# Optimization experiments

Measured on AMD Instinct MI355X. Metric: run time of the kernel, lower is better.

Reference implementation:

```python
import jax, jax.numpy as jnp
import numpy as np

N_NODES = 100000


def _segment_mean(h, src, dst, n_nodes):
    # copy_u: gather source features along edges, then mean-reduce per dst node
    msg = h[src]                                             # [E, D]
    s = jax.ops.segment_sum(msg, dst, num_segments=n_nodes)  # [N, D]
    cnt = jax.ops.segment_sum(jnp.ones((src.shape[0],), h.dtype), dst,
                              num_segments=n_nodes)          # [N]
    return s / jnp.maximum(cnt, 1.0)[:, None]


def setup_inputs() -> dict:
    key = jax.random.key(0)
    k1, k2, k3, k4, k5 = jax.random.split(key, 5)
    in_feats, n_hidden, n_classes = 128, 128, 64
    n_edges = 1600000
    features = jax.random.normal(k1, (N_NODES, in_feats), dtype=jnp.float32)
    W1 = jax.random.normal(k2, (in_feats, n_hidden), dtype=jnp.float32) * (1.0 / np.sqrt(in_feats))
    b1 = jnp.zeros((n_hidden,), jnp.float32)
    W2 = jax.random.normal(k3, (n_hidden, n_classes), dtype=jnp.float32) * (1.0 / np.sqrt(n_hidden))
    b2 = jnp.zeros((n_classes,), jnp.float32)
    src = jax.random.randint(k4, (n_edges,), 0, N_NODES, dtype=jnp.int64)
    dst = jax.random.randint(k5, (n_edges,), 0, N_NODES, dtype=jnp.int64)
    return {"features": features, "W1": W1, "b1": b1, "W2": W2, "b2": b2,
            "src": src, "dst": dst}


def reference(features, W1, b1, W2, b2, src, dst):
    # Layer 0: mean aggregation -> Linear -> relu  (dropout p=0.0 is identity)
    h = _segment_mean(features, src, dst, N_NODES)
    h = jax.nn.relu(h @ W1 + b1)
    # Layer 1: mean aggregation -> Linear (no activation on output layer)
    h = _segment_mean(h, src, dst, N_NODES)
    h = h @ W2 + b2
    return h
```

## Files before the change

kernel.cpp:

```cpp
#include <hip/hip_runtime.h>

#define N_NODES 100000
#define D 128
#define NE 1600000
#define C_OUT 64
#define NB 391
#define SENT 100000
#define P2B 256
#define P2E 6250
#define SEGSTRIDE 6400

typedef _Float16 half8 __attribute__((ext_vector_type(8)));
typedef float floatx4 __attribute__((ext_vector_type(4)));


__device__ inline half8 shfl_xor_h8(half8 v, int mask) {
    union { half8 h; int i[4]; } u;
    u.h = v;
    u.i[0] = __shfl_xor(u.i[0], mask);
    u.i[1] = __shfl_xor(u.i[1], mask);
    u.i[2] = __shfl_xor(u.i[2], mask);
    u.i[3] = __shfl_xor(u.i[3], mask);
    return u.h;
}

__device__ inline void pack_one(const float* W, _Float16* Wp, int tid, int N) {
    int l = tid & 63, p = tid >> 6;
    int nt = p >> 2, kc = p & 3;
    int quad = l >> 4, c = l & 15;
    int n = nt * 16 + c;
    half8 h;
    #pragma unroll
    for (int j = 0; j < 8; ++j) {
        int k = kc * 32 + quad * 8 + j;
        h[j] = (_Float16)W[k * N + n];
    }
    *(half8*)(Wp + (size_t)p * 512 + l * 8) = h;
}

__global__ __launch_bounds__(1024) void k1_p2_setup(const int* __restrict__ src,
                                                    const int* __restrict__ dst,
                                                    unsigned* __restrict__ gwords,
                                                    int* __restrict__ ofsg,
                                                    const float* __restrict__ W1,
                                                    const float* __restrict__ W2,
                                                    _Float16* __restrict__ wp1,
                                                    _Float16* __restrict__ wp2,
                                                    int* __restrict__ t1s,
                                                    int* __restrict__ t2s) {
    if (blockIdx.x >= P2B) {
        const int blk = blockIdx.x - P2B;
        const int t = threadIdx.x;
        if (t < 256) {
            if (blk < 8) {
                pack_one(W1, wp1, blk * 256 + t, 128);
            } else if (blk < 12) {
                pack_one(W2, wp2, (blk - 8) * 256 + t, 64);
            } else {
                if (t < 64) t1s[t] = 0;
                else if (t < 96) t2s[t - 64] = 0;
            }
        }
        return;
    }

    __shared__ unsigned ebuf[P2E];
    __shared__ int hist[NB];
    __shared__ int ofs[NB + 1];
    __shared__ int cur[NB];
    __shared__ int wsum[8];
    const int t = threadIdx.x;
    const int base = blockIdx.x * P2E;

    for (int i = t; i < NB; i += 1024) hist[i] = 0;
    __syncthreads();

    unsigned w[7];
    int bk[7];
    #pragma unroll
    for (int r = 0; r < 7; ++r) {
        const int j = r * 1024 + t;
        if (j < P2E) {
            const int e = base + j;
            const int d = dst[e];
            w[r] = ((unsigned)(d & 255) << 20) | (unsigned)src[e];
            bk[r] = d >> 8;
            atomicAdd(&hist[bk[r]], 1);
        } else {
            bk[r] = -1;
        }
    }
    __syncthreads();

    int v = 0, incl = 0;
    if (t < 512) { v = (t < NB) ? hist[t] : 0; incl = v; }
    #pragma unroll
    for (int d = 1; d < 64; d <<= 1) {
        int y = __shfl_up(incl, d);
        if ((t & 63) >= d) incl += y;
    }
    if (t < 512 && (t & 63) == 63) wsum[t >> 6] = incl;
    __syncthreads();
    if (t < NB) {
        int ex = incl - v;
        const int wv = t >> 6;
        for (int j = 0; j < wv; ++j) ex += wsum[j];
        ofs[t] = ex;
        cur[t] = ex;
    }
    if (t == 0) ofs[NB] = P2E;
    __syncthreads();

    #pragma unroll
    for (int r = 0; r < 7; ++r) {
        if (bk[r] >= 0) {
            const int slot = atomicAdd(&cur[bk[r]], 1);
            ebuf[slot] = w[r];
        }
    }
    __syncthreads();

    unsigned* gout = gwords + (size_t)blockIdx.x * SEGSTRIDE;
    for (int i = t; i < P2E; i += 1024) gout[i] = ebuf[i];
    int* oout = ofsg + blockIdx.x * (NB + 1);
    for (int i = t; i < NB + 1; i += 1024) oout[i] = ofs[i];
}

__global__ __launch_bounds__(256) void k2_p3_gemm1(const unsigned* __restrict__ gwords,
                                                   const int* __restrict__ ofsg,
                                                   int* __restrict__ ptrp,
                                                   int* __restrict__ pcnt,
                                                   float* __restrict__ inv,
                                                   int* __restrict__ csr,
                                                   const float* __restrict__ A,
                                                   const _Float16* __restrict__ Wp,
                                                   _Float16* __restrict__ outh) {
    __shared__ __align__(16) char smem[40960];
    const int t = threadIdx.x;

    if (blockIdx.x < NB) {
        unsigned* wbuf = (unsigned*)smem;
        int* sa   = (int*)(smem + 32768);
        int* sl   = (int*)(smem + 33792);
        int* so   = (int*)(smem + 34816);
        int* lcnt = (int*)(smem + 35840);
        int* lofs = (int*)(smem + 36864);
        int* ws4  = (int*)(smem + 37888);
        const int b = blockIdx.x;
        const int lane = t & 63, wave = t >> 6;

        const int* row = ofsg + t * (NB + 1);
        const int a0 = row[b];
        const int len = row[b + 1] - a0;
        sa[t] = a0;
        sl[t] = len;

        int sv = a0;
        #pragma unroll
        for (int m2 = 1; m2 < 64; m2 <<= 1) sv += __shfl_xor(sv, m2);
        if (lane == 0) ws4[wave] = sv;
        __syncthreads();
        const int pad_base = (ws4[0] + ws4[1] + ws4[2] + ws4[3]) + 1792 * b;
        __syncthreads();

        int incl = len;
        #pragma unroll
        for (int d = 1; d < 64; d <<= 1) {
            int y = __shfl_up(incl, d);
            if (lane >= d) incl += y;
        }
        if (lane == 63) ws4[wave] = incl;
        lcnt[t] = 0;
        __syncthreads();
        int off = incl - len;
        for (int j = 0; j < wave; ++j) off += ws4[j];
        so[t] = off;
        const int tot = min(ws4[0] + ws4[1] + ws4[2] + ws4[3], 8192);
        __syncthreads();

        const int grp = t >> 4, gl = t & 15;
        for (int seg = grp; seg < P2B; seg += 16) {
            const int sega = sa[seg];
            const int segl = sl[seg];
            const int sego = so[seg];
            if (sego + segl > 8192) continue;
            const unsigned* sp = gwords + (size_t)seg * SEGSTRIDE + sega;
            for (int j = gl; j < segl; j += 16) {
                const unsigned w = sp[j];
                wbuf[sego + j] = w;
                atomicAdd(&lcnt[(w >> 20) & 255], 1);
            }
        }
        __syncthreads();

        const int v = lcnt[t];
        const int pc = (v + 7) & ~7;
        int incl2 = pc;
        #pragma unroll
        for (int d = 1; d < 64; d <<= 1) {
            int y = __shfl_up(incl2, d);
            if (lane >= d) incl2 += y;
        }
        __syncthreads();
        if (lane == 63) ws4[wave] = incl2;
        __syncthreads();
        int ex = incl2 - pc;
        for (int j = 0; j < wave; ++j) ex += ws4[j];

        const int node = b * 256 + t;
        if (node < N_NODES) {
            ptrp[node] = pad_base + ex;
            pcnt[node] = pc;
            inv[node] = 1.0f / fmaxf((float)v, 1.0f);
        }
        for (int j = v; j < pc; ++j) csr[pad_base + ex + j] = SENT;

        __syncthreads();
        lofs[t] = ex;
        __syncthreads();
        for (int i = t; i < tot; i += 256) {
            const unsigned w = wbuf[i];
            const int pos = atomicAdd(&lofs[(w >> 20) & 255], 1);
            csr[pad_base + pos] = (int)(w & 0xFFFFF);
        }
        return;
    }

    _Float16* Wl = (_Float16*)smem;
    _Float16* Al = (_Float16*)(smem + 32768);
    {
        const floatx4* s4 = (const floatx4*)Wp;
        floatx4* d4 = (floatx4*)Wl;
        #pragma unroll
        for (int i = 0; i < 8; ++i) d4[t + 256 * i] = s4[t + 256 * i];
    }
    const int lane = t & 63;
    const int wave = t >> 6;
    const int row0 = (blockIdx.x - NB) * 128;

    floatx4 acc[8][2];
    #pragma unroll
    for (int mt = 0; mt < 8; ++mt)
        #pragma unroll
        for (int nt = 0; nt < 2; ++nt) acc[mt][nt] = (floatx4)0.0f;

    for (int kc = 0; kc < 4; ++kc) {
        __syncthreads();
        #pragma unroll
        for (int rep = 0; rep < 2; ++rep) {
            int p = rep * 256 + t;
            int r = p >> 2, quad = p & 3;
            int row = row0 + r;
            if (row > N_NODES - 1) row = N_NODES - 1;
            const float4 x0 = *(const float4*)(A + (size_t)row * D + kc * 32 + quad * 8);
            const float4 x1 = *(const float4*)(A + (size_t)row * D + kc * 32 + quad * 8 + 4);
            half8 h;
            h[0] = (_Float16)x0.x; h[1] = (_Float16)x0.y;
            h[2] = (_Float16)x0.z; h[3] = (_Float16)x0.w;
            h[4] = (_Float16)x1.x; h[5] = (_Float16)x1.y;
            h[6] = (_Float16)x1.z; h[7] = (_Float16)x1.w;
            int mt = r >> 4, m = r & 15;
            *(half8*)(Al + mt * 512 + (quad * 16 + m) * 8) = h;
        }
        __syncthreads();
        const half8* Af = (const half8*)Al;
        const half8* Bf = (const half8*)Wl;
        half8 b0 = Bf[((wave * 2 + 0) * 4 + kc) * 64 + lane];
        half8 b1 = Bf[((wave * 2 + 1) * 4 + kc) * 64 + lane];
        #pragma unroll
        for (int mt = 0; mt < 8; ++mt) {
            half8 a = Af[mt * 64 + lane];
            acc[mt][0] = __builtin_amdgcn_mfma_f32_16x16x32_f16(a, b0, acc[mt][0], 0, 0, 0);
            acc[mt][1] = __builtin_amdgcn_mfma_f32_16x16x32_f16(a, b1, acc[mt][1], 0, 0, 0);
        }
    }

    const int quad = lane >> 4, cl = lane & 15;
    #pragma unroll
    for (int mt = 0; mt < 8; ++mt)
        #pragma unroll
        for (int nt = 0; nt < 2; ++nt) {
            int col = wave * 32 + nt * 16 + cl;
            #pragma unroll
            for (int i = 0; i < 4; ++i) {
                int row = row0 + mt * 16 + quad * 4 + i;
                if (row < N_NODES)
                    outh[(size_t)row * D + col] = (_Float16)acc[mt][nt][i];
            }
        }
}

__global__ __launch_bounds__(256) void kF_agg_gemm2(const _Float16* __restrict__ f,
                                                    const int* __restrict__ ptrp,
                                                    const int* __restrict__ pcnt,
                                                    const int* __restrict__ csr,
                                                    const float* __restrict__ inv,
                                                    const float* __restrict__ bias,
                                                    const _Float16* __restrict__ Wp,
                                                    _Float16* __restrict__ outh) {
    __shared__ __align__(16) _Float16 Wl[8192];
    __shared__ __align__(16) _Float16 h1t[16 * 136];
    const int t = threadIdx.x;
    {
        const floatx4* s4 = (const floatx4*)Wp;
        floatx4* d4 = (floatx4*)Wl;
        #pragma unroll
        for (int i = 0; i < 4; ++i) d4[t + 256 * i] = s4[t + 256 * i];
    }
    const int wave = t >> 6;
    const int lane = t & 63;
    const int q = lane & 15, hf = lane >> 4;
    const half8* f8 = (const half8*)f;

    for (int it = 0; it < 4; ++it) {
        const int r = wave * 4 + it;
        const int n = blockIdx.x * 16 + r;
        const int begin = ptrp[n];
        const int end = begin + pcnt[n];
        const float iv = inv[n];

        half8 acc0 = {0, 0, 0, 0, 0, 0, 0, 0};
        half8 acc1 = {0, 0, 0, 0, 0, 0, 0, 0};
        for (int base = begin; base < end; base += 64) {
            const int m = min(64, end - base);
            int edge = (lane < m) ? csr[base + lane] : SENT;
            int i = 0;
            for (; i + 16 <= m; i += 16) {
                int s0 = __shfl(edge, i + hf);
                int s1 = __shfl(edge, i + 4 + hf);
                int s2 = __shfl(edge, i + 8 + hf);
                int s3 = __shfl(edge, i + 12 + hf);
                half8 v0 = f8[(size_t)s0 * 16 + q];
                half8 v1 = f8[(size_t)s1 * 16 + q];
                half8 v2 = f8[(size_t)s2 * 16 + q];
                half8 v3 = f8[(size_t)s3 * 16 + q];
                acc0 += v0;
                acc1 += v1;
                acc0 += v2;
                acc1 += v3;
            }
            if (i < m) {
                int s0 = __shfl(edge, i + hf);
                int s1 = __shfl(edge, i + 4 + hf);
                half8 v0 = f8[(size_t)s0 * 16 + q];
                half8 v1 = f8[(size_t)s1 * 16 + q];
                acc0 += v0;
                acc1 += v1;
            }
        }
        acc0 += acc1;
        acc0 += shfl_xor_h8(acc0, 16);
        acc0 += shfl_xor_h8(acc0, 32);
        if (hf == 0) {
            const float4 b0 = ((const float4*)bias)[q * 2];
            const float4 b1v = ((const float4*)bias)[q * 2 + 1];
            half8 o;
            o[0] = (_Float16)fmaxf((float)acc0[0] * iv + b0.x, 0.f);
            o[1] = (_Float16)fmaxf((float)acc0[1] * iv + b0.y, 0.f);
            o[2] = (_Float16)fmaxf((float)acc0[2] * iv + b0.z, 0.f);
            o[3] = (_Float16)fmaxf((float)acc0[3] * iv + b0.w, 0.f);
            o[4] = (_Float16)fmaxf((float)acc0[4] * iv + b1v.x, 0.f);
            o[5] = (_Float16)fmaxf((float)acc0[5] * iv + b1v.y, 0.f);
            o[6] = (_Float16)fmaxf((float)acc0[6] * iv + b1v.z, 0.f);
            o[7] = (_Float16)fmaxf((float)acc0[7] * iv + b1v.w, 0.f);
            *(half8*)(h1t + r * 136 + q * 8) = o;
        }
    }
    __syncthreads();

    floatx4 acc = (floatx4)0.0f;
    #pragma unroll
    for (int kc = 0; kc < 4; ++kc) {
        half8 a = *(const half8*)(h1t + (lane & 15) * 136 + kc * 32 + (lane >> 4) * 8);
        half8 b = ((const half8*)Wl)[(wave * 4 + kc) * 64 + lane];
        acc = __builtin_amdgcn_mfma_f32_16x16x32_f16(a, b, acc, 0, 0, 0);
    }
    const int quad = lane >> 4, cl = lane & 15;
    const int col = wave * 16 + cl;
    #pragma unroll
    for (int i = 0; i < 4; ++i) {
        const int row = blockIdx.x * 16 + quad * 4 + i;
        outh[(size_t)row * C_OUT + col] = (_Float16)acc[i];
    }
}

__global__ __launch_bounds__(256) void kG_agg64(const _Float16* __restrict__ f,
                                                const int* __restrict__ ptrp,
                                                const int* __restrict__ pcnt,
                                                const int* __restrict__ csr,
                                                const float* __restrict__ inv,
                                                const float* __restrict__ bias,
                                                float* __restrict__ out) {
    const int wave = threadIdx.x >> 6;
    const int lane = threadIdx.x & 63;
    const int q = lane & 7, hf = lane >> 3;
    const int n = blockIdx.x * 4 + wave;
    const int begin = ptrp[n];
    const int end = begin + pcnt[n];
    const float iv = inv[n];
    const half8* f8 = (const half8*)f;

    half8 acc0 = {0, 0, 0, 0, 0, 0, 0, 0};
    half8 acc1 = {0, 0, 0, 0, 0, 0, 0, 0};
    for (int base = begin; base < end; base += 64) {
        const int m = min(64, end - base);
        int edge = (lane < m) ? csr[base + lane] : SENT;
        int i = 0;
        for (; i + 32 <= m; i += 32) {
            int s0 = __shfl(edge, i + hf);
            int s1 = __shfl(edge, i + 8 + hf);
            int s2 = __shfl(edge, i + 16 + hf);
            int s3 = __shfl(edge, i + 24 + hf);
            half8 v0 = f8[(size_t)s0 * 8 + q];
            half8 v1 = f8[(size_t)s1 * 8 + q];
            half8 v2 = f8[(size_t)s2 * 8 + q];
            half8 v3 = f8[(size_t)s3 * 8 + q];
            acc0 += v0;
            acc1 += v1;
            acc0 += v2;
            acc1 += v3;
        }
        if (i + 16 <= m) {
            int s0 = __shfl(edge, i + hf);
            int s1 = __shfl(edge, i + 8 + hf);
            half8 v0 = f8[(size_t)s0 * 8 + q];
            half8 v1 = f8[(size_t)s1 * 8 + q];
            acc0 += v0;
            acc1 += v1;
            i += 16;
        }
        if (i < m) {
            int s = __shfl(edge, i + hf);
            acc0 += f8[(size_t)s * 8 + q];
        }
    }
    acc0 += acc1;
    acc0 += shfl_xor_h8(acc0, 8);
    acc0 += shfl_xor_h8(acc0, 16);
    acc0 += shfl_xor_h8(acc0, 32);
    if (hf == 0) {
        const float4 b0 = ((const float4*)bias)[q * 2];
        const float4 b1 = ((const float4*)bias)[q * 2 + 1];
        float4 o0, o1;
        o0.x = (float)acc0[0] * iv + b0.x;
        o0.y = (float)acc0[1] * iv + b0.y;
        o0.z = (float)acc0[2] * iv + b0.z;
        o0.w = (float)acc0[3] * iv + b0.w;
        o1.x = (float)acc0[4] * iv + b1.x;
        o1.y = (float)acc0[5] * iv + b1.y;
        o1.z = (float)acc0[6] * iv + b1.z;
        o1.w = (float)acc0[7] * iv + b1.w;
        ((float4*)out)[(size_t)n * 16 + q * 2] = o0;
        ((float4*)out)[(size_t)n * 16 + q * 2 + 1] = o1;
    }
}

extern "C" void kernel_launch(void* const* d_in, const int* in_sizes, int n_in,
                              void* d_out, int out_size, void* d_ws, size_t ws_size,
                              hipStream_t stream) {
    const float* features = (const float*)d_in[0];
    const float* W1 = (const float*)d_in[1];
    const float* b1 = (const float*)d_in[2];
    const float* W2 = (const float*)d_in[3];
    const float* b2 = (const float*)d_in[4];
    const int* src = (const int*)d_in[5];
    const int* dst = (const int*)d_in[6];
    float* out = (float*)d_out;

    char* ws = (char*)d_ws;
    int*      ofsg  = (int*)(ws + 512L * 4);
    int*      ptrp  = (int*)(ws + 125952L * 4);
    int*      pcnt  = (int*)(ws + 225952L * 4);
    float*    inv   = (float*)(ws + 325952L * 4);
    int*      csr   = (int*)(ws + 425952L * 4);
    unsigned* gwords= (unsigned*)(ws + 2825952L * 4);
    _Float16* wp1   = (_Float16*)(ws + 4464352L * 4);
    _Float16* wp2   = (_Float16*)(ws + 4472544L * 4);
    _Float16* t1h   = (_Float16*)(ws + 4476640L * 4);
    _Float16* t2h   = (_Float16*)(ws + 17276704L * 4);

    k1_p2_setup<<<P2B + 13, 1024, 0, stream>>>(src, dst, gwords, ofsg, W1, W2, wp1, wp2,
                                               (int*)(t1h + (size_t)SENT * 128),
                                               (int*)(t2h + (size_t)SENT * 64));
    k2_p3_gemm1<<<NB + 782, 256, 0, stream>>>(gwords, ofsg, ptrp, pcnt, inv, csr,
                                              features, wp1, t1h);
    kF_agg_gemm2<<<N_NODES / 16, 256, 0, stream>>>(t1h, ptrp, pcnt, csr, inv, b1, wp2, t2h);
    kG_agg64<<<N_NODES / 4, 256, 0, stream>>>(t2h, ptrp, pcnt, csr, inv, b2, out);
}
```

Baseline: 227.4 us.

## Widen fused CSR-build/GEMM1 kernel to 1024-thread blocks sharing one W tile

Changes the combined CSR-build and first GEMM kernel from 256-thread to 1024-thread blocks. In the CSR partition blocks, the extra threads help with segment gathering and scatter, while the scans stay on the first 256 threads. In the GEMM blocks, four 128-row subtiles share a single shared-memory copy of packed W1, which cuts redundant weight loads and the GEMM block count from 782 to 196. The cost is larger blocks with more shared memory, and therefore possibly lower occupancy. The sub-tiles also now share block-wide barriers.

```diff
diff --git a/kernel.cpp b/kernel.cpp
--- a/kernel.cpp
+++ b/kernel.cpp
@@ -9,6 +9,7 @@
 #define P2B 256
 #define P2E 6250
 #define SEGSTRIDE 6400
+#define GEMM1_QUADS 196
 
 typedef _Float16 half8 __attribute__((ext_vector_type(8)));
 typedef float floatx4 __attribute__((ext_vector_type(4)));
@@ -126,16 +127,16 @@
     for (int i = t; i < NB + 1; i += 1024) oout[i] = ofs[i];
 }
 
-__global__ __launch_bounds__(256) void k2_p3_gemm1(const unsigned* __restrict__ gwords,
-                                                   const int* __restrict__ ofsg,
-                                                   int* __restrict__ ptrp,
-                                                   int* __restrict__ pcnt,
-                                                   float* __restrict__ inv,
-                                                   int* __restrict__ csr,
-                                                   const float* __restrict__ A,
-                                                   const _Float16* __restrict__ Wp,
-                                                   _Float16* __restrict__ outh) {
-    __shared__ __align__(16) char smem[40960];
+__global__ __launch_bounds__(1024) void k2_p3_gemm1(const unsigned* __restrict__ gwords,
+                                                    const int* __restrict__ ofsg,
+                                                    int* __restrict__ ptrp,
+                                                    int* __restrict__ pcnt,
+                                                    float* __restrict__ inv,
+                                                    int* __restrict__ csr,
+                                                    const float* __restrict__ A,
+                                                    const _Float16* __restrict__ Wp,
+                                                    _Float16* __restrict__ outh) {
+    __shared__ __align__(16) char smem[65536];
     const int t = threadIdx.x;
 
     if (blockIdx.x < NB) {
@@ -146,40 +147,48 @@
         int* lcnt = (int*)(smem + 35840);
         int* lofs = (int*)(smem + 36864);
         int* ws4  = (int*)(smem + 37888);
+        int* shv  = (int*)(smem + 37904);
         const int b = blockIdx.x;
         const int lane = t & 63, wave = t >> 6;
 
-        const int* row = ofsg + t * (NB + 1);
-        const int a0 = row[b];
-        const int len = row[b + 1] - a0;
-        sa[t] = a0;
-        sl[t] = len;
-
-        int sv = a0;
-        #pragma unroll
-        for (int m2 = 1; m2 < 64; m2 <<= 1) sv += __shfl_xor(sv, m2);
-        if (lane == 0) ws4[wave] = sv;
-        __syncthreads();
-        const int pad_base = (ws4[0] + ws4[1] + ws4[2] + ws4[3]) + 1792 * b;
-        __syncthreads();
-
-        int incl = len;
-        #pragma unroll
-        for (int d = 1; d < 64; d <<= 1) {
-            int y = __shfl_up(incl, d);
-            if (lane >= d) incl += y;
-        }
-        if (lane == 63) ws4[wave] = incl;
-        lcnt[t] = 0;
-        __syncthreads();
-        int off = incl - len;
-        for (int j = 0; j < wave; ++j) off += ws4[j];
-        so[t] = off;
-        const int tot = min(ws4[0] + ws4[1] + ws4[2] + ws4[3], 8192);
+        if (t < 256) {
+            const int* row = ofsg + t * (NB + 1);
+            const int a0 = row[b];
+            const int len = row[b + 1] - a0;
+            sa[t] = a0;
+            sl[t] = len;
+            lcnt[t] = 0;
+            int sv = a0;
+            #pragma unroll
+            for (int m2 = 1; m2 < 64; m2 <<= 1) sv += __shfl_xor(sv, m2);
+            if (lane == 0) ws4[wave] = sv;
+        }
+        __syncthreads();
+        if (t == 0) shv[0] = ws4[0] + ws4[1] + ws4[2] + ws4[3] + 1792 * b;
+        __syncthreads();
+
+        int incl = 0, mylen = 0;
+        if (t < 256) {
+            mylen = sl[t];
+            incl = mylen;
+            #pragma unroll
+            for (int d = 1; d < 64; d <<= 1) {
+                int y = __shfl_up(incl, d);
+                if (lane >= d) incl += y;
+            }
+            if (lane == 63) ws4[wave] = incl;
+        }
+        __syncthreads();
+        if (t < 256) {
+            int off = incl - mylen;
+            for (int j = 0; j < wave; ++j) off += ws4[j];
+            so[t] = off;
+        }
+        if (t == 0) shv[1] = min(ws4[0] + ws4[1] + ws4[2] + ws4[3], 8192);
         __syncthreads();
 
         const int grp = t >> 4, gl = t & 15;
-        for (int seg = grp; seg < P2B; seg += 16) {
+        for (int seg = grp; seg < P2B; seg += 64) {
             const int sega = sa[seg];
             const int segl = sl[seg];
             const int sego = so[seg];
@@ -193,32 +202,36 @@
         }
         __syncthreads();
 
-        const int v = lcnt[t];
-        const int pc = (v + 7) & ~7;
-        int incl2 = pc;
-        #pragma unroll
-        for (int d = 1; d < 64; d <<= 1) {
-            int y = __shfl_up(incl2, d);
-            if (lane >= d) incl2 += y;
-        }
-        __syncthreads();
-        if (lane == 63) ws4[wave] = incl2;
-        __syncthreads();
-        int ex = incl2 - pc;
-        for (int j = 0; j < wave; ++j) ex += ws4[j];
-
-        const int node = b * 256 + t;
-        if (node < N_NODES) {
-            ptrp[node] = pad_base + ex;
-            pcnt[node] = pc;
-            inv[node] = 1.0f / fmaxf((float)v, 1.0f);
-        }
-        for (int j = v; j < pc; ++j) csr[pad_base + ex + j] = SENT;
-
-        __syncthreads();
-        lofs[t] = ex;
-        __syncthreads();
-        for (int i = t; i < tot; i += 256) {
+        const int pad_base = shv[0];
+        int ex = 0, v = 0, pc = 0;
+        if (t < 256) {
+            v = lcnt[t];
+            pc = (v + 7) & ~7;
+            int incl2 = pc;
+            #pragma unroll
+            for (int d = 1; d < 64; d <<= 1) {
+                int y = __shfl_up(incl2, d);
+                if (lane >= d) incl2 += y;
+            }
+            if (lane == 63) ws4[wave] = incl2;
+            ex = incl2 - pc;
+        }
+        __syncthreads();
+        if (t < 256) {
+            for (int j = 0; j < wave; ++j) ex += ws4[j];
+            const int node = b * 256 + t;
+            if (node < N_NODES) {
+                ptrp[node] = pad_base + ex;
+                pcnt[node] = pc;
+                inv[node] = 1.0f / fmaxf((float)v, 1.0f);
+            }
+            for (int j = v; j < pc; ++j) csr[pad_base + ex + j] = SENT;
+            lofs[t] = ex;
+        }
+        __syncthreads();
+
+        const int tot = shv[1];
+        for (int i = t; i < tot; i += 1024) {
             const unsigned w = wbuf[i];
             const int pos = atomicAdd(&lofs[(w >> 20) & 255], 1);
             csr[pad_base + pos] = (int)(w & 0xFFFFF);
@@ -227,16 +240,18 @@
     }
 
     _Float16* Wl = (_Float16*)smem;
-    _Float16* Al = (_Float16*)(smem + 32768);
+    _Float16* Al = (_Float16*)(smem + 32768) + (t >> 8) * 4096;
+    const int sub = t >> 8;
+    const int tid = t & 255;
     {
         const floatx4* s4 = (const floatx4*)Wp;
         floatx4* d4 = (floatx4*)Wl;
         #pragma unroll
-        for (int i = 0; i < 8; ++i) d4[t + 256 * i] = s4[t + 256 * i];
-    }
-    const int lane = t & 63;
-    const int wave = t >> 6;
-    const int row0 = (blockIdx.x - NB) * 128;
+        for (int i = 0; i < 2; ++i) d4[t + 1024 * i] = s4[t + 1024 * i];
+    }
+    const int lane = tid & 63;
+    const int wave = tid >> 6;
+    const int row0 = ((blockIdx.x - NB) * 4 + sub) * 128;
 
     floatx4 acc[8][2];
     #pragma unroll
@@ -248,7 +263,7 @@
         __syncthreads();
         #pragma unroll
         for (int rep = 0; rep < 2; ++rep) {
-            int p = rep * 256 + t;
+            int p = rep * 256 + tid;
             int r = p >> 2, quad = p & 3;
             int row = row0 + r;
             if (row > N_NODES - 1) row = N_NODES - 1;
@@ -482,8 +497,8 @@
     k1_p2_setup<<<P2B + 13, 1024, 0, stream>>>(src, dst, gwords, ofsg, W1, W2, wp1, wp2,
                                                (int*)(t1h + (size_t)SENT * 128),
                                                (int*)(t2h + (size_t)SENT * 64));
-    k2_p3_gemm1<<<NB + 782, 256, 0, stream>>>(gwords, ofsg, ptrp, pcnt, inv, csr,
-                                              features, wp1, t1h);
+    k2_p3_gemm1<<<NB + GEMM1_QUADS, 1024, 0, stream>>>(gwords, ofsg, ptrp, pcnt, inv, csr,
+                                                       features, wp1, t1h);
     kF_agg_gemm2<<<N_NODES / 16, 256, 0, stream>>>(t1h, ptrp, pcnt, csr, inv, b1, wp2, t2h);
     kG_agg64<<<N_NODES / 4, 256, 0, stream>>>(t2h, ptrp, pcnt, csr, inv, b2, out);
 }
```

Measured after the change: 231.8 us. No clear change (+1.9%).
